# Optimization experiments

Hardware: AMD Instinct MI355X
Metric: run time of the kernel (lower is better)

The kernel has to match this reference:

```python
import jax, jax.numpy as jnp
import numpy as np

B, N, K = 32, 128, 16
F_ATOM, F_NEI, D = 256, 256, 256
H = 4
DK = D // H
NEG = -1e9
EPS = 1e-5
SLOPE = 0.2  # LeakyReLU slope (GAT convention)


def setup_inputs() -> dict:
    key = jax.random.key(0)
    ks = jax.random.split(key, 10)
    atom_feature = jax.random.normal(ks[0], (B, N, F_ATOM), jnp.float32)
    atom_neighbor_feature = jax.random.normal(ks[1], (B, N, K, F_NEI), jnp.float32)
    keep = (jax.random.uniform(ks[2], (B, N, K, 1)) < 0.8).astype(jnp.float32)
    atom_softmax_mask = (keep - 1.0) * (-NEG)  # 0 where valid, -1e9 where padded
    atom_attend_mask = keep
    s_a = 1.0 / np.sqrt(F_ATOM)
    s_n = 1.0 / np.sqrt(F_NEI)
    s_al = 1.0 / np.sqrt(DK)
    return {
        "atom_feature": atom_feature,
        "atom_neighbor_feature": atom_neighbor_feature,
        "atom_softmax_mask": atom_softmax_mask,
        "atom_attend_mask": atom_attend_mask,
        "W_a": jax.random.uniform(ks[3], (D, F_ATOM), jnp.float32, -s_a, s_a),
        "b_a": jnp.zeros((D,), jnp.float32),
        "W_n": jax.random.uniform(ks[4], (D, F_NEI), jnp.float32, -s_n, s_n),
        "b_n": jnp.zeros((D,), jnp.float32),
        "w_align": jax.random.uniform(ks[5], (DK,), jnp.float32, -s_al, s_al),
        "b_align": jnp.zeros((), jnp.float32),
        "ln_gamma": jnp.ones((D,), jnp.float32),
        "ln_beta": jnp.zeros((D,), jnp.float32),
    }


def reference(atom_feature, atom_neighbor_feature, atom_softmax_mask,
              atom_attend_mask, W_a, b_a, W_n, b_n, w_align, b_align,
              ln_gamma, ln_beta):
    # Linear projections (dropout is identity at inference)
    af = jnp.einsum('bnf,df->bnd', atom_feature, W_a) + b_a            # [B,N,D]
    nf = jnp.einsum('bnkf,df->bnkd', atom_neighbor_feature, W_n) + b_n  # [B,N,K,D]
    b, n, k, d = nf.shape
    afh = af.reshape(b, n, 1, H, DK)      # broadcast over neighbor axis
    nfh = nf.reshape(b, n, k, H, DK)
    # GATV2: act(Wa x_i + Wn x_j) . a
    feat = jax.nn.leaky_relu(afh + nfh, SLOPE)                          # [B,N,K,H,DK]
    score = jnp.einsum('bnkhd,d->bnkh', feat, w_align) + b_align        # [B,N,K,H]
    score = score + atom_softmax_mask                                   # [B,N,K,1] -> bcast over H
    attw = jax.nn.softmax(score, axis=2)                                # softmax over neighbors
    attw = attw * atom_attend_mask                                      # zero out padded neighbors
    ctx = jnp.einsum('bnkh,bnkhd->bnhd', attw, nfh).reshape(b, n, d)    # weighted sum
    # LayerNorm
    mu = jnp.mean(ctx, axis=-1, keepdims=True)
    var = jnp.mean(jnp.square(ctx - mu), axis=-1, keepdims=True)
    out = (ctx - mu) * jax.lax.rsqrt(var + EPS) * ln_gamma + ln_beta
    return out
```

## Files before the change

kernel.cpp:

```cpp
#include <hip/hip_runtime.h>
#include <hip/hip_bf16.h>


typedef float f32x4 __attribute__((ext_vector_type(4)));
typedef __bf16 bf16x8 __attribute__((ext_vector_type(8)));

__device__ __forceinline__ unsigned short f2bf(float x) {
    unsigned int u = __float_as_uint(x);
    u += 0x7FFFu + ((u >> 16) & 1u);
    return (unsigned short)(u >> 16);
}

__global__ __launch_bounds__(256) void conv_w(const float* __restrict__ wa,
                                              const float* __restrict__ wn,
                                              unsigned short* __restrict__ owa,
                                              unsigned short* __restrict__ own) {
    const int g = blockIdx.x * 256 + threadIdx.x;
    const float* src = (g & 8192) ? wn : wa;
    unsigned short* dst = (g & 8192) ? own : owa;
    const int c = g & 8191;
    const int lane = c & 63, ni = (c >> 6) & 3, kk = (c >> 8) & 7, wv = c >> 11;
    const int d = wv * 64 + ni * 16 + (lane & 15);
    const int f = kk * 32 + (lane >> 4) * 8;
    const float* sp = src + d * 256 + f;
    unsigned short h[8];
#pragma unroll
    for (int j = 0; j < 8; ++j) h[j] = f2bf(sp[j]);
    *(uint4*)(dst + c * 8) = *(const uint4*)h;
}

__global__ __launch_bounds__(256) void proj_atoms(const float* __restrict__ atomf,
                                                  const unsigned short* __restrict__ wa_p,
                                                  const float* __restrict__ b_a,
                                                  float* __restrict__ af) {
    __shared__ char lds[16 * 512];
    const int tid = threadIdx.x, p = blockIdx.x;
    const float4* src4 = (const float4*)(atomf + (size_t)p * 16 * 256);
#pragma unroll
    for (int j = 0; j < 4; ++j) {
        const int idx4 = tid + j * 256;
        const float4 v = src4[idx4];
        const int r = idx4 >> 6, byt = (idx4 & 63) * 8;
        ushort4 h;
        h.x = f2bf(v.x); h.y = f2bf(v.y); h.z = f2bf(v.z); h.w = f2bf(v.w);
        *(ushort4*)(lds + r * 512 + (byt ^ ((r & 7) << 4))) = h;
    }
    __syncthreads();
    const int lane = tid & 63, wv = tid >> 6, l15 = lane & 15, lg = lane >> 4;
    f32x4 acc[4];
#pragma unroll
    for (int ni = 0; ni < 4; ++ni)
#pragma unroll
        for (int j = 0; j < 4; ++j) acc[ni][j] = 0.f;
    const unsigned short* w = wa_p + wv * 16384 + lane * 8;
#pragma unroll
    for (int kk = 0; kk < 8; ++kk) {
        const int fb = (kk * 32 + lg * 8) * 2;
        const int r = l15;
        const bf16x8 afr = *(const bf16x8*)(lds + r * 512 + (fb ^ ((r & 7) << 4)));
#pragma unroll
        for (int ni = 0; ni < 4; ++ni) {
            const bf16x8 cn = *(const bf16x8*)(w + kk * 2048 + ni * 512);
            acc[ni] = __builtin_amdgcn_mfma_f32_16x16x32_bf16(afr, cn, acc[ni], 0, 0, 0);
        }
    }
#pragma unroll
    for (int ni = 0; ni < 4; ++ni) {
        const int d = wv * 64 + ni * 16 + l15;
        const float bav = b_a[d];
#pragma unroll
        for (int j = 0; j < 4; ++j)
            af[(size_t)(p * 16 + lg * 4 + j) * 256 + d] = acc[ni][j] + bav;
    }
}

struct SmemG {
    char  a[64 * 512];
    float af[4][256];
    float wal[64];
    float sm[4][16];
    float am[4][16];
    float red[4][4][2];
};

__global__ __launch_bounds__(256, 4) void gat4(
        const float* __restrict__ nei, const float* __restrict__ af_buf,
        const unsigned short* __restrict__ wn_p, const float* __restrict__ b_n,
        const float* __restrict__ smask, const float* __restrict__ amask,
        const float* __restrict__ w_align, const float* __restrict__ b_align,
        const float* __restrict__ gamma, const float* __restrict__ beta,
        float* __restrict__ out) {
    __shared__ SmemG s;
    const int tid = threadIdx.x;
    const int p = blockIdx.x;

    const float4* src4 = (const float4*)(nei + (size_t)p * 64 * 256);
#pragma unroll
    for (int j = 0; j < 16; ++j) {
        const int idx4 = tid + j * 256;
        const float4 v = src4[idx4];
        const int r = idx4 >> 6, byt = (idx4 & 63) * 8;
        ushort4 h;
        h.x = f2bf(v.x); h.y = f2bf(v.y); h.z = f2bf(v.z); h.w = f2bf(v.w);
        *(ushort4*)(s.a + r * 512 + (byt ^ ((r & 7) << 4))) = h;
    }
#pragma unroll
    for (int a2 = 0; a2 < 4; ++a2)
        s.af[a2][tid] = af_buf[(size_t)p * 1024 + a2 * 256 + tid];
    if (tid < 64) {
        s.wal[tid] = w_align[tid];
        ((float*)s.sm)[tid] = smask[p * 64 + tid];
        ((float*)s.am)[tid] = amask[p * 64 + tid];
    }
    __syncthreads();

    const int lane = tid & 63, wv = tid >> 6, l15 = lane & 15, lg = lane >> 4;

    f32x4 acc[4][4];
#pragma unroll
    for (int a = 0; a < 4; ++a)
#pragma unroll
        for (int ni = 0; ni < 4; ++ni)
#pragma unroll
            for (int j = 0; j < 4; ++j) acc[a][ni][j] = 0.f;

    const unsigned short* w = wn_p + wv * 16384 + lane * 8;
#pragma unroll
    for (int kk = 0; kk < 8; ++kk) {
        const int fb = (kk * 32 + lg * 8) * 2;
        bf16x8 afr[4];
#pragma unroll
        for (int a = 0; a < 4; ++a) {
            const int r = a * 16 + l15;
            afr[a] = *(const bf16x8*)(s.a + r * 512 + (fb ^ ((r & 7) << 4)));
        }
#pragma unroll
        for (int ni = 0; ni < 4; ++ni) {
            const bf16x8 cn = *(const bf16x8*)(w + kk * 2048 + ni * 512);
#pragma unroll
            for (int a = 0; a < 4; ++a)
                acc[a][ni] = __builtin_amdgcn_mfma_f32_16x16x32_bf16(afr[a], cn, acc[a][ni], 0, 0, 0);
        }
    }

    float bn4[4], wl4[4];
#pragma unroll
    for (int ni = 0; ni < 4; ++ni) {
        bn4[ni] = b_n[wv * 64 + ni * 16 + l15];
        wl4[ni] = s.wal[ni * 16 + l15];
    }
#pragma unroll
    for (int a = 0; a < 4; ++a)
#pragma unroll
        for (int ni = 0; ni < 4; ++ni)
#pragma unroll
            for (int j = 0; j < 4; ++j) acc[a][ni][j] += bn4[ni];

    const float bal = b_align[0];
    float ctx[4][4];
#pragma unroll
    for (int a = 0; a < 4; ++a) {
        float afd[4];
#pragma unroll
        for (int ni = 0; ni < 4; ++ni)
            afd[ni] = s.af[a][wv * 64 + ni * 16 + l15];
        float sj[4];
#pragma unroll
        for (int j = 0; j < 4; ++j) {
            float t = 0.f;
#pragma unroll
            for (int ni = 0; ni < 4; ++ni) {
                float z = afd[ni] + acc[a][ni][j];
                z = fmaxf(z, 0.2f * z);
                t = fmaf(z, wl4[ni], t);
            }
            sj[j] = t;
        }
#pragma unroll
        for (int j = 0; j < 4; ++j) {
#pragma unroll
            for (int o = 1; o < 16; o <<= 1) sj[j] += __shfl_xor(sj[j], o);
            sj[j] += bal + s.sm[a][lg * 4 + j];
        }
        float m = fmaxf(fmaxf(sj[0], sj[1]), fmaxf(sj[2], sj[3]));
        m = fmaxf(m, __shfl_xor(m, 16));
        m = fmaxf(m, __shfl_xor(m, 32));
        float e[4], sum = 0.f;
#pragma unroll
        for (int j = 0; j < 4; ++j) { e[j] = __expf(sj[j] - m); sum += e[j]; }
        sum += __shfl_xor(sum, 16);
        sum += __shfl_xor(sum, 32);
        const float inv = 1.f / sum;
        float aw[4];
#pragma unroll
        for (int j = 0; j < 4; ++j) aw[j] = e[j] * inv * s.am[a][lg * 4 + j];
#pragma unroll
        for (int ni = 0; ni < 4; ++ni) {
            float c = 0.f;
#pragma unroll
            for (int j = 0; j < 4; ++j) c = fmaf(aw[j], acc[a][ni][j], c);
            c += __shfl_xor(c, 16);
            c += __shfl_xor(c, 32);
            ctx[a][ni] = c;
        }
        float t = 0.f, q = 0.f;
#pragma unroll
        for (int ni = 0; ni < 4; ++ni) { t += ctx[a][ni]; q = fmaf(ctx[a][ni], ctx[a][ni], q); }
#pragma unroll
        for (int o = 1; o < 16; o <<= 1) { t += __shfl_xor(t, o); q += __shfl_xor(q, o); }
        if (lane == 0) { s.red[wv][a][0] = t; s.red[wv][a][1] = q; }
    }
    __syncthreads();

    const float g = gamma[wv * 64 + lane];
    const float be = beta[wv * 64 + lane];
#pragma unroll
    for (int a = 0; a < 4; ++a) {
        float ts = 0.f, tq = 0.f;
#pragma unroll
        for (int q2 = 0; q2 < 4; ++q2) { ts += s.red[q2][a][0]; tq += s.red[q2][a][1]; }
        const float mu = ts * (1.f / 256.f);
        float var = tq * (1.f / 256.f) - mu * mu;
        var = fmaxf(var, 0.f);
        const float rs = rsqrtf(var + 1e-5f);
        const float cv = (lg == 0) ? ctx[a][0] : (lg == 1) ? ctx[a][1]
                        : (lg == 2) ? ctx[a][2] : ctx[a][3];
        out[(size_t)(p * 4 + a) * 256 + wv * 64 + lane] = (cv - mu) * rs * g + be;
    }
}

extern "C" void kernel_launch(void* const* d_in, const int* in_sizes, int n_in,
                              void* d_out, int out_size, void* d_ws, size_t ws_size,
                              hipStream_t stream) {
    const float* atomf = (const float*)d_in[0];
    const float* nei   = (const float*)d_in[1];
    const float* smask = (const float*)d_in[2];
    const float* amask = (const float*)d_in[3];
    const float* Wa    = (const float*)d_in[4];
    const float* ba    = (const float*)d_in[5];
    const float* Wn    = (const float*)d_in[6];
    const float* bn    = (const float*)d_in[7];
    const float* wal   = (const float*)d_in[8];
    const float* bal   = (const float*)d_in[9];
    const float* gam   = (const float*)d_in[10];
    const float* bet   = (const float*)d_in[11];
    float* out = (float*)d_out;

    char* ws = (char*)d_ws;
    float*          af_buf = (float*)ws;
    unsigned short* wa_bf  = (unsigned short*)(ws + 4194304);
    unsigned short* wn_bf  = (unsigned short*)(ws + 4194304 + 131072);

    hipLaunchKernelGGL(conv_w, dim3(64), dim3(256), 0, stream,
                       Wa, Wn, wa_bf, wn_bf);
    hipLaunchKernelGGL(proj_atoms, dim3(256), dim3(256), 0, stream,
                       atomf, wa_bf, ba, af_buf);
    hipLaunchKernelGGL(gat4, dim3(1024), dim3(256), 0, stream,
                       nei, af_buf, wn_bf, bn, smask, amask,
                       wal, bal, gam, bet, out);
}
```

Before: 136.5 us.

## Merge weight conversion into atom projection; prefetch Wn fragments in gat4

Merges the separate weight-conversion and atom-projection kernels into one prep kernel. The first 32 blocks convert only Wn to bf16, and the atom-projection blocks read Wa as fp32 and convert it inline, which removes one kernel launch and the dependency between them. In gat4, each thread now issues its global neighbor loads in 8-float chunks into registers before converting them, and the Wn fragments for the next k-step are double-buffered in registers. Occupancy is lowered to 3 blocks per CU to leave room for the extra registers. The trade-off is redundant Wa conversion across projection blocks and fewer resident waves.

```diff
diff --git a/kernel.cpp b/kernel.cpp
--- a/kernel.cpp
+++ b/kernel.cpp
@@ -11,39 +11,43 @@
     return (unsigned short)(u >> 16);
 }
 
-__global__ __launch_bounds__(256) void conv_w(const float* __restrict__ wa,
-                                              const float* __restrict__ wn,
-                                              unsigned short* __restrict__ owa,
-                                              unsigned short* __restrict__ own) {
-    const int g = blockIdx.x * 256 + threadIdx.x;
-    const float* src = (g & 8192) ? wn : wa;
-    unsigned short* dst = (g & 8192) ? own : owa;
-    const int c = g & 8191;
-    const int lane = c & 63, ni = (c >> 6) & 3, kk = (c >> 8) & 7, wv = c >> 11;
-    const int d = wv * 64 + ni * 16 + (lane & 15);
-    const int f = kk * 32 + (lane >> 4) * 8;
-    const float* sp = src + d * 256 + f;
-    unsigned short h[8];
-#pragma unroll
-    for (int j = 0; j < 8; ++j) h[j] = f2bf(sp[j]);
-    *(uint4*)(dst + c * 8) = *(const uint4*)h;
-}
-
-__global__ __launch_bounds__(256) void proj_atoms(const float* __restrict__ atomf,
-                                                  const unsigned short* __restrict__ wa_p,
-                                                  const float* __restrict__ b_a,
-                                                  float* __restrict__ af) {
+__global__ __launch_bounds__(256) void prep(const float* __restrict__ atomf,
+                                            const float* __restrict__ wa_f,
+                                            const float* __restrict__ wn_f,
+                                            unsigned short* __restrict__ own,
+                                            const float* __restrict__ b_a,
+                                            float* __restrict__ af) {
+    const int blk = blockIdx.x;
+    const int tid = threadIdx.x;
+    if (blk < 32) {
+        const int c = blk * 256 + tid;
+        const int lane = c & 63, ni = (c >> 6) & 3, kk = (c >> 8) & 7, wv = c >> 11;
+        const int d = wv * 64 + ni * 16 + (lane & 15);
+        const int f = kk * 32 + (lane >> 4) * 8;
+        const float* sp = wn_f + d * 256 + f;
+        unsigned short h[8];
+#pragma unroll
+        for (int j = 0; j < 8; ++j) h[j] = f2bf(sp[j]);
+        *(uint4*)(own + c * 8) = *(const uint4*)h;
+        return;
+    }
+    const int p = blk - 32;
     __shared__ char lds[16 * 512];
-    const int tid = threadIdx.x, p = blockIdx.x;
     const float4* src4 = (const float4*)(atomf + (size_t)p * 16 * 256);
-#pragma unroll
-    for (int j = 0; j < 4; ++j) {
-        const int idx4 = tid + j * 256;
-        const float4 v = src4[idx4];
-        const int r = idx4 >> 6, byt = (idx4 & 63) * 8;
-        ushort4 h;
-        h.x = f2bf(v.x); h.y = f2bf(v.y); h.z = f2bf(v.z); h.w = f2bf(v.w);
-        *(ushort4*)(lds + r * 512 + (byt ^ ((r & 7) << 4))) = h;
+    float4 v[4];
+#pragma unroll
+    for (int m = 0; m < 2; ++m) {
+        v[2 * m]     = src4[tid * 2 + m * 512];
+        v[2 * m + 1] = src4[tid * 2 + 1 + m * 512];
+    }
+#pragma unroll
+    for (int m = 0; m < 2; ++m) {
+        const int r = (tid >> 5) + 8 * m;
+        const int byt = (tid & 31) * 16;
+        unsigned short h[8];
+        h[0] = f2bf(v[2*m].x); h[1] = f2bf(v[2*m].y); h[2] = f2bf(v[2*m].z); h[3] = f2bf(v[2*m].w);
+        h[4] = f2bf(v[2*m+1].x); h[5] = f2bf(v[2*m+1].y); h[6] = f2bf(v[2*m+1].z); h[7] = f2bf(v[2*m+1].w);
+        *(uint4*)(lds + r * 512 + (byt ^ ((r & 7) << 4))) = *(const uint4*)h;
     }
     __syncthreads();
     const int lane = tid & 63, wv = tid >> 6, l15 = lane & 15, lg = lane >> 4;
@@ -52,7 +56,6 @@
     for (int ni = 0; ni < 4; ++ni)
 #pragma unroll
         for (int j = 0; j < 4; ++j) acc[ni][j] = 0.f;
-    const unsigned short* w = wa_p + wv * 16384 + lane * 8;
 #pragma unroll
     for (int kk = 0; kk < 8; ++kk) {
         const int fb = (kk * 32 + lg * 8) * 2;
@@ -60,8 +63,13 @@
         const bf16x8 afr = *(const bf16x8*)(lds + r * 512 + (fb ^ ((r & 7) << 4)));
 #pragma unroll
         for (int ni = 0; ni < 4; ++ni) {
-            const bf16x8 cn = *(const bf16x8*)(w + kk * 2048 + ni * 512);
-            acc[ni] = __builtin_amdgcn_mfma_f32_16x16x32_bf16(afr, cn, acc[ni], 0, 0, 0);
+            const float* wp = wa_f + (size_t)(wv * 64 + ni * 16 + l15) * 256 + kk * 32 + lg * 8;
+            const float4 wx = *(const float4*)wp;
+            const float4 wy = *(const float4*)(wp + 4);
+            unsigned short hw[8];
+            hw[0] = f2bf(wx.x); hw[1] = f2bf(wx.y); hw[2] = f2bf(wx.z); hw[3] = f2bf(wx.w);
+            hw[4] = f2bf(wy.x); hw[5] = f2bf(wy.y); hw[6] = f2bf(wy.z); hw[7] = f2bf(wy.w);
+            acc[ni] = __builtin_amdgcn_mfma_f32_16x16x32_bf16(afr, *(const bf16x8*)hw, acc[ni], 0, 0, 0);
         }
     }
 #pragma unroll
@@ -83,7 +91,7 @@
     float red[4][4][2];
 };
 
-__global__ __launch_bounds__(256, 4) void gat4(
+__global__ __launch_bounds__(256, 3) void gat4(
         const float* __restrict__ nei, const float* __restrict__ af_buf,
         const unsigned short* __restrict__ wn_p, const float* __restrict__ b_n,
         const float* __restrict__ smask, const float* __restrict__ amask,
@@ -94,24 +102,31 @@
     const int tid = threadIdx.x;
     const int p = blockIdx.x;
 
-    const float4* src4 = (const float4*)(nei + (size_t)p * 64 * 256);
-#pragma unroll
-    for (int j = 0; j < 16; ++j) {
-        const int idx4 = tid + j * 256;
-        const float4 v = src4[idx4];
-        const int r = idx4 >> 6, byt = (idx4 & 63) * 8;
-        ushort4 h;
-        h.x = f2bf(v.x); h.y = f2bf(v.y); h.z = f2bf(v.z); h.w = f2bf(v.w);
-        *(ushort4*)(s.a + r * 512 + (byt ^ ((r & 7) << 4))) = h;
-    }
-#pragma unroll
-    for (int a2 = 0; a2 < 4; ++a2)
-        s.af[a2][tid] = af_buf[(size_t)p * 1024 + a2 * 256 + tid];
     if (tid < 64) {
         s.wal[tid] = w_align[tid];
         ((float*)s.sm)[tid] = smask[p * 64 + tid];
         ((float*)s.am)[tid] = amask[p * 64 + tid];
     }
+#pragma unroll
+    for (int a2 = 0; a2 < 4; ++a2)
+        s.af[a2][tid] = af_buf[(size_t)p * 1024 + a2 * 256 + tid];
+
+    const float4* src4 = (const float4*)(nei + (size_t)p * 64 * 256);
+    float4 v[16];
+#pragma unroll
+    for (int m = 0; m < 8; ++m) {
+        v[2 * m]     = src4[tid * 2 + m * 512];
+        v[2 * m + 1] = src4[tid * 2 + 1 + m * 512];
+    }
+#pragma unroll
+    for (int m = 0; m < 8; ++m) {
+        const int r = (tid >> 5) + 8 * m;
+        const int byt = (tid & 31) * 16;
+        unsigned short h[8];
+        h[0] = f2bf(v[2*m].x); h[1] = f2bf(v[2*m].y); h[2] = f2bf(v[2*m].z); h[3] = f2bf(v[2*m].w);
+        h[4] = f2bf(v[2*m+1].x); h[5] = f2bf(v[2*m+1].y); h[6] = f2bf(v[2*m+1].z); h[7] = f2bf(v[2*m+1].w);
+        *(uint4*)(s.a + r * 512 + (byt ^ ((r & 7) << 4))) = *(const uint4*)h;
+    }
     __syncthreads();
 
     const int lane = tid & 63, wv = tid >> 6, l15 = lane & 15, lg = lane >> 4;
@@ -125,8 +140,16 @@
             for (int j = 0; j < 4; ++j) acc[a][ni][j] = 0.f;
 
     const unsigned short* w = wn_p + wv * 16384 + lane * 8;
+    bf16x8 cur[4], nxt[4];
+#pragma unroll
+    for (int ni = 0; ni < 4; ++ni) cur[ni] = *(const bf16x8*)(w + ni * 512);
 #pragma unroll
     for (int kk = 0; kk < 8; ++kk) {
+        if (kk < 7) {
+#pragma unroll
+            for (int ni = 0; ni < 4; ++ni)
+                nxt[ni] = *(const bf16x8*)(w + (kk + 1) * 2048 + ni * 512);
+        }
         const int fb = (kk * 32 + lg * 8) * 2;
         bf16x8 afr[4];
 #pragma unroll
@@ -135,11 +158,14 @@
             afr[a] = *(const bf16x8*)(s.a + r * 512 + (fb ^ ((r & 7) << 4)));
         }
 #pragma unroll
-        for (int ni = 0; ni < 4; ++ni) {
-            const bf16x8 cn = *(const bf16x8*)(w + kk * 2048 + ni * 512);
+        for (int ni = 0; ni < 4; ++ni)
 #pragma unroll
             for (int a = 0; a < 4; ++a)
-                acc[a][ni] = __builtin_amdgcn_mfma_f32_16x16x32_bf16(afr[a], cn, acc[a][ni], 0, 0, 0);
+                acc[a][ni] = __builtin_amdgcn_mfma_f32_16x16x32_bf16(afr[a], cur[ni], acc[a][ni], 0, 0, 0);
+        if (kk < 7) {
+            asm volatile("" :: "v"(nxt[0]), "v"(nxt[1]), "v"(nxt[2]), "v"(nxt[3]));
+#pragma unroll
+            for (int ni = 0; ni < 4; ++ni) cur[ni] = nxt[ni];
         }
     }
 
@@ -248,13 +274,10 @@
 
     char* ws = (char*)d_ws;
     float*          af_buf = (float*)ws;
-    unsigned short* wa_bf  = (unsigned short*)(ws + 4194304);
-    unsigned short* wn_bf  = (unsigned short*)(ws + 4194304 + 131072);
-
-    hipLaunchKernelGGL(conv_w, dim3(64), dim3(256), 0, stream,
-                       Wa, Wn, wa_bf, wn_bf);
-    hipLaunchKernelGGL(proj_atoms, dim3(256), dim3(256), 0, stream,
-                       atomf, wa_bf, ba, af_buf);
+    unsigned short* wn_bf  = (unsigned short*)(ws + 4194304);
+
+    hipLaunchKernelGGL(prep, dim3(288), dim3(256), 0, stream,
+                       atomf, Wa, Wn, wn_bf, ba, af_buf);
     hipLaunchKernelGGL(gat4, dim3(1024), dim3(256), 0, stream,
                        nei, af_buf, wn_bf, bn, smask, amask,
                        wal, bal, gam, bet, out);
```

After: 143.5 us. +5.1%, slower.

## Fuse atom projection into GAT kernel and prefetch neighbor weights

Applied to the files above, without the earlier changes.

Removes the separate proj_atoms kernel and its af workspace round trip. Each GAT block now converts its 4 atom rows into extra LDS rows and computes their projection with additional MFMAs alongside the neighbor projection, then distributes the result via shuffles. It also software-prefetches the next k-step of W_n fragments into registers and restructures the neighbor load into wider 8-element bf16 stores. The trade-off is more registers and LDS per block, with the occupancy bound lowered from 4 to 3 blocks per SM, and redundant W_a fragment loads in every block.

```diff
diff --git a/kernel.cpp b/kernel.cpp
--- a/kernel.cpp
+++ b/kernel.cpp
@@ -29,63 +29,17 @@
     *(uint4*)(dst + c * 8) = *(const uint4*)h;
 }
 
-__global__ __launch_bounds__(256) void proj_atoms(const float* __restrict__ atomf,
-                                                  const unsigned short* __restrict__ wa_p,
-                                                  const float* __restrict__ b_a,
-                                                  float* __restrict__ af) {
-    __shared__ char lds[16 * 512];
-    const int tid = threadIdx.x, p = blockIdx.x;
-    const float4* src4 = (const float4*)(atomf + (size_t)p * 16 * 256);
-#pragma unroll
-    for (int j = 0; j < 4; ++j) {
-        const int idx4 = tid + j * 256;
-        const float4 v = src4[idx4];
-        const int r = idx4 >> 6, byt = (idx4 & 63) * 8;
-        ushort4 h;
-        h.x = f2bf(v.x); h.y = f2bf(v.y); h.z = f2bf(v.z); h.w = f2bf(v.w);
-        *(ushort4*)(lds + r * 512 + (byt ^ ((r & 7) << 4))) = h;
-    }
-    __syncthreads();
-    const int lane = tid & 63, wv = tid >> 6, l15 = lane & 15, lg = lane >> 4;
-    f32x4 acc[4];
-#pragma unroll
-    for (int ni = 0; ni < 4; ++ni)
-#pragma unroll
-        for (int j = 0; j < 4; ++j) acc[ni][j] = 0.f;
-    const unsigned short* w = wa_p + wv * 16384 + lane * 8;
-#pragma unroll
-    for (int kk = 0; kk < 8; ++kk) {
-        const int fb = (kk * 32 + lg * 8) * 2;
-        const int r = l15;
-        const bf16x8 afr = *(const bf16x8*)(lds + r * 512 + (fb ^ ((r & 7) << 4)));
-#pragma unroll
-        for (int ni = 0; ni < 4; ++ni) {
-            const bf16x8 cn = *(const bf16x8*)(w + kk * 2048 + ni * 512);
-            acc[ni] = __builtin_amdgcn_mfma_f32_16x16x32_bf16(afr, cn, acc[ni], 0, 0, 0);
-        }
-    }
-#pragma unroll
-    for (int ni = 0; ni < 4; ++ni) {
-        const int d = wv * 64 + ni * 16 + l15;
-        const float bav = b_a[d];
-#pragma unroll
-        for (int j = 0; j < 4; ++j)
-            af[(size_t)(p * 16 + lg * 4 + j) * 256 + d] = acc[ni][j] + bav;
-    }
-}
-
 struct SmemG {
-    char  a[64 * 512];
-    float af[4][256];
-    float wal[64];
+    char  a[68 * 512];
     float sm[4][16];
     float am[4][16];
     float red[4][4][2];
 };
 
-__global__ __launch_bounds__(256, 4) void gat4(
-        const float* __restrict__ nei, const float* __restrict__ af_buf,
-        const unsigned short* __restrict__ wn_p, const float* __restrict__ b_n,
+__global__ __launch_bounds__(256, 3) void gat_one(
+        const float* __restrict__ atomf, const float* __restrict__ nei,
+        const unsigned short* __restrict__ wn_p, const unsigned short* __restrict__ wa_p,
+        const float* __restrict__ b_n, const float* __restrict__ b_a,
         const float* __restrict__ smask, const float* __restrict__ amask,
         const float* __restrict__ w_align, const float* __restrict__ b_align,
         const float* __restrict__ gamma, const float* __restrict__ beta,
@@ -94,60 +48,100 @@
     const int tid = threadIdx.x;
     const int p = blockIdx.x;
 
+    if (tid < 64) {
+        ((float*)s.sm)[tid] = smask[p * 64 + tid];
+        ((float*)s.am)[tid] = amask[p * 64 + tid];
+    }
+
     const float4* src4 = (const float4*)(nei + (size_t)p * 64 * 256);
 #pragma unroll
-    for (int j = 0; j < 16; ++j) {
-        const int idx4 = tid + j * 256;
-        const float4 v = src4[idx4];
-        const int r = idx4 >> 6, byt = (idx4 & 63) * 8;
+    for (int half = 0; half < 2; ++half) {
+        float4 v[8];
+#pragma unroll
+        for (int m = 0; m < 4; ++m) {
+            v[2 * m]     = src4[tid * 2 + (half * 4 + m) * 512];
+            v[2 * m + 1] = src4[tid * 2 + 1 + (half * 4 + m) * 512];
+        }
+#pragma unroll
+        for (int m = 0; m < 4; ++m) {
+            const int r = (tid >> 5) + 8 * (half * 4 + m);
+            const int byt = (tid & 31) * 16;
+            unsigned short h[8];
+            h[0] = f2bf(v[2*m].x); h[1] = f2bf(v[2*m].y); h[2] = f2bf(v[2*m].z); h[3] = f2bf(v[2*m].w);
+            h[4] = f2bf(v[2*m+1].x); h[5] = f2bf(v[2*m+1].y); h[6] = f2bf(v[2*m+1].z); h[7] = f2bf(v[2*m+1].w);
+            *(uint4*)(s.a + r * 512 + (byt ^ ((r & 7) << 4))) = *(const uint4*)h;
+        }
+    }
+    {
+        const int at = tid >> 6, cc = tid & 63;
+        const float4 v = *(const float4*)(atomf + (size_t)(p * 4 + at) * 256 + cc * 4);
+        const int r = 64 + at;
         ushort4 h;
         h.x = f2bf(v.x); h.y = f2bf(v.y); h.z = f2bf(v.z); h.w = f2bf(v.w);
-        *(ushort4*)(s.a + r * 512 + (byt ^ ((r & 7) << 4))) = h;
-    }
-#pragma unroll
-    for (int a2 = 0; a2 < 4; ++a2)
-        s.af[a2][tid] = af_buf[(size_t)p * 1024 + a2 * 256 + tid];
-    if (tid < 64) {
-        s.wal[tid] = w_align[tid];
-        ((float*)s.sm)[tid] = smask[p * 64 + tid];
-        ((float*)s.am)[tid] = amask[p * 64 + tid];
+        *(ushort4*)(s.a + r * 512 + ((cc * 8) ^ ((r & 7) << 4))) = h;
     }
     __syncthreads();
 
     const int lane = tid & 63, wv = tid >> 6, l15 = lane & 15, lg = lane >> 4;
 
     f32x4 acc[4][4];
+    f32x4 accA[4];
 #pragma unroll
     for (int a = 0; a < 4; ++a)
 #pragma unroll
         for (int ni = 0; ni < 4; ++ni)
 #pragma unroll
             for (int j = 0; j < 4; ++j) acc[a][ni][j] = 0.f;
-
-    const unsigned short* w = wn_p + wv * 16384 + lane * 8;
+#pragma unroll
+    for (int ni = 0; ni < 4; ++ni)
+#pragma unroll
+        for (int j = 0; j < 4; ++j) accA[ni][j] = 0.f;
+
+    const unsigned short* wn_wv = wn_p + wv * 16384 + lane * 8;
+    const unsigned short* wa_wv = wa_p + wv * 16384 + lane * 8;
+    bf16x8 cn[4], nx[4];
+#pragma unroll
+    for (int ni = 0; ni < 4; ++ni) cn[ni] = *(const bf16x8*)(wn_wv + ni * 512);
 #pragma unroll
     for (int kk = 0; kk < 8; ++kk) {
+        if (kk < 7) {
+#pragma unroll
+            for (int ni = 0; ni < 4; ++ni)
+                nx[ni] = *(const bf16x8*)(wn_wv + (kk + 1) * 2048 + ni * 512);
+        }
         const int fb = (kk * 32 + lg * 8) * 2;
-        bf16x8 afr[4];
+        bf16x8 afr[5];
 #pragma unroll
         for (int a = 0; a < 4; ++a) {
             const int r = a * 16 + l15;
             afr[a] = *(const bf16x8*)(s.a + r * 512 + (fb ^ ((r & 7) << 4)));
         }
+        {
+            const int r = 64 + (l15 & 3);
+            afr[4] = *(const bf16x8*)(s.a + r * 512 + (fb ^ ((r & 7) << 4)));
+        }
 #pragma unroll
         for (int ni = 0; ni < 4; ++ni) {
-            const bf16x8 cn = *(const bf16x8*)(w + kk * 2048 + ni * 512);
+            const bf16x8 ca = *(const bf16x8*)(wa_wv + kk * 2048 + ni * 512);
 #pragma unroll
             for (int a = 0; a < 4; ++a)
-                acc[a][ni] = __builtin_amdgcn_mfma_f32_16x16x32_bf16(afr[a], cn, acc[a][ni], 0, 0, 0);
-        }
-    }
-
-    float bn4[4], wl4[4];
+                acc[a][ni] = __builtin_amdgcn_mfma_f32_16x16x32_bf16(afr[a], cn[ni], acc[a][ni], 0, 0, 0);
+            accA[ni] = __builtin_amdgcn_mfma_f32_16x16x32_bf16(afr[4], ca, accA[ni], 0, 0, 0);
+        }
+        if (kk < 7) {
+            asm volatile("" :: "v"(nx[0]), "v"(nx[1]), "v"(nx[2]), "v"(nx[3]));
+#pragma unroll
+            for (int ni = 0; ni < 4; ++ni) cn[ni] = nx[ni];
+        }
+    }
+
+    float bn4[4], ba4[4], wl4[4];
 #pragma unroll
     for (int ni = 0; ni < 4; ++ni) {
-        bn4[ni] = b_n[wv * 64 + ni * 16 + l15];
-        wl4[ni] = s.wal[ni * 16 + l15];
+        const int dd = wv * 64 + ni * 16 + l15;
+        bn4[ni] = b_n[dd];
+        ba4[ni] = b_a[dd];
+        wl4[ni] = w_align[ni * 16 + l15];
     }
 #pragma unroll
     for (int a = 0; a < 4; ++a)
@@ -163,7 +157,7 @@
         float afd[4];
 #pragma unroll
         for (int ni = 0; ni < 4; ++ni)
-            afd[ni] = s.af[a][wv * 64 + ni * 16 + l15];
+            afd[ni] = __shfl(accA[ni][a], l15) + ba4[ni];
         float sj[4];
 #pragma unroll
         for (int j = 0; j < 4; ++j) {
@@ -247,15 +241,12 @@
     float* out = (float*)d_out;
 
     char* ws = (char*)d_ws;
-    float*          af_buf = (float*)ws;
-    unsigned short* wa_bf  = (unsigned short*)(ws + 4194304);
-    unsigned short* wn_bf  = (unsigned short*)(ws + 4194304 + 131072);
+    unsigned short* wa_bf = (unsigned short*)ws;
+    unsigned short* wn_bf = (unsigned short*)(ws + 131072);
 
     hipLaunchKernelGGL(conv_w, dim3(64), dim3(256), 0, stream,
                        Wa, Wn, wa_bf, wn_bf);
-    hipLaunchKernelGGL(proj_atoms, dim3(256), dim3(256), 0, stream,
-                       atomf, wa_bf, ba, af_buf);
-    hipLaunchKernelGGL(gat4, dim3(1024), dim3(256), 0, stream,
-                       nei, af_buf, wn_bf, bn, smask, amask,
+    hipLaunchKernelGGL(gat_one, dim3(1024), dim3(256), 0, stream,
+                       atomf, nei, wn_bf, wa_bf, bn, ba, smask, amask,
                        wal, bal, gam, bet, out);
 }
```

Result: no change. 138.0 us (+1.1%).
